# Performance work log

Hardware: AMD Instinct MI355X
Metric: run time of the kernel (lower is better)

The kernel has to match this reference:

```python
import jax, jax.numpy as jnp
import numpy as np
from jax import lax

B, C, H, W = 4, 256, 64, 64
R = 4  # reduction
BN_EPS = 1e-5


def setup_inputs() -> dict:
    key = jax.random.key(0)
    ks = jax.random.split(key, 18)
    n = jax.random.normal
    return {
        "x_self": n(ks[0], (B, C, H, W), jnp.float32),
        "x_other": n(ks[1], (B, C, H, W), jnp.float32),
        "q_w": n(ks[2], (C, C), jnp.float32) * 0.05,      # self_q 1x1 conv
        "q_b": n(ks[3], (C,), jnp.float32) * 0.05,
        "kv_w": n(ks[4], (2 * C, C), jnp.float32) * 0.05,  # other_kv 1x1 conv
        "kv_b": n(ks[5], (2 * C,), jnp.float32) * 0.05,
        "g1_w": n(ks[6], (C // R, C), jnp.float32) * 0.05,  # gate conv1
        "g1_b": n(ks[7], (C // R,), jnp.float32) * 0.05,
        "g2_w": n(ks[8], (1, C // R), jnp.float32) * 0.05,  # gate conv2
        "g2_b": n(ks[9], (1,), jnp.float32) * 0.05,
        "dw_w": n(ks[10], (C, 1, 3, 3), jnp.float32) * 0.1,  # depthwise 3x3
        "dw_b": n(ks[11], (C,), jnp.float32) * 0.05,
        "bn_g": jnp.ones((C,), jnp.float32),
        "bn_b": jnp.zeros((C,), jnp.float32),
        "bn_m": n(ks[12], (C,), jnp.float32) * 0.05,
        "bn_v": jax.random.uniform(ks[13], (C,), jnp.float32, 0.5, 1.5),
        "out_w": n(ks[14], (C, C), jnp.float32) * 0.05,
        "out_b": n(ks[15], (C,), jnp.float32) * 0.05,
    }


def _conv1x1(x, w, b):
    return jnp.einsum('bchw,oc->bohw', x, w) + b[None, :, None, None]


def reference(x_self, x_other, q_w, q_b, kv_w, kv_b, g1_w, g1_b, g2_w, g2_b,
              dw_w, dw_b, bn_g, bn_b, bn_m, bn_v, out_w, out_b):
    # local branch: depthwise 3x3 conv -> BatchNorm (eval stats) -> SiLU
    y = lax.conv_general_dilated(
        x_self, dw_w, (1, 1), 'SAME',
        feature_group_count=C,
        dimension_numbers=('NCHW', 'OIHW', 'NCHW')) + dw_b[None, :, None, None]
    scale = (bn_g / jnp.sqrt(bn_v + BN_EPS))[None, :, None, None]
    y = (y - bn_m[None, :, None, None]) * scale + bn_b[None, :, None, None]
    local_feat = y * jax.nn.sigmoid(y)  # SiLU

    # cross attention over HW tokens
    q = _conv1x1(x_self, q_w, q_b).reshape(B, C, H * W)
    kv = _conv1x1(x_other, kv_w, kv_b)
    k = kv[:, :C].reshape(B, C, H * W)
    v = kv[:, C:].reshape(B, C, H * W)
    attn = jnp.einsum('bcn,bcm->bnm', q, k) / jnp.sqrt(jnp.float32(C))  # [B,HW,HW]
    attn = jax.nn.softmax(attn, axis=-1)
    attn_out = jnp.einsum('bnm,bcm->bcn', attn, v).reshape(B, C, H, W)

    # channel-squeeze gate on x_self -> scalar per sample
    p = jnp.mean(x_self, axis=(2, 3))                 # [B,C] global avg pool
    g = jax.nn.relu(p @ g1_w.T + g1_b)                # [B,C//R]
    g = jax.nn.sigmoid(g @ g2_w.T + g2_b)             # [B,1]
    gate = g[:, :, None, None]

    fused = local_feat + gate * attn_out
    return _conv1x1(fused, out_w, out_b)
```

## Files before the change

### kernel.cpp

```cpp
#include <hip/hip_runtime.h>
#include <stdint.h>

#define BB 4
#define CC 256
#define HH 64
#define WWD 64
#define NN 4096
#define LOG2E 1.4426950408889634f

typedef __attribute__((ext_vector_type(8))) short short8;
typedef __attribute__((ext_vector_type(4))) float f32x4;
typedef __attribute__((ext_vector_type(16))) float f32x16;
typedef __attribute__((ext_vector_type(4))) unsigned short us4;
typedef unsigned long long ull;

__device__ __forceinline__ unsigned short f2bf(float f) {
  unsigned int u = __float_as_uint(f);
  u += 0x7fffu + ((u >> 16) & 1u);
  return (unsigned short)(u >> 16);
}
__device__ __forceinline__ float bf2f(unsigned short h) {
  return __uint_as_float(((unsigned int)h) << 16);
}
__device__ __forceinline__ short8 ld8(const unsigned short* p) {
  return *reinterpret_cast<const short8*>(p);
}
__device__ __forceinline__ unsigned char f2fp8(float v) {
  return (unsigned char)__builtin_amdgcn_cvt_pk_fp8_f32(v, v, 0, false);
}
__device__ __forceinline__ int rowmap(int reg, int h) {
  return (reg & 3) + 8 * (reg >> 2) + 4 * h;
}
__device__ __forceinline__ void gll16(const void* g, void* l) {
  __builtin_amdgcn_global_load_lds(
      (const __attribute__((address_space(1))) unsigned int*)g,
      (__attribute__((address_space(3))) unsigned int*)l, 16, 0, 0);
}

__global__ __launch_bounds__(256, 2) void k_pre(
    const float* __restrict__ xs, const float* __restrict__ xo,
    const float* __restrict__ dww, const float* __restrict__ dwb,
    const float* __restrict__ bng, const float* __restrict__ bnb,
    const float* __restrict__ bnm, const float* __restrict__ bnv,
    const float* __restrict__ qw, const float* __restrict__ kvw,
    const float* __restrict__ ow, unsigned short* __restrict__ XtS,
    unsigned short* __restrict__ XtO, unsigned short* __restrict__ localT,
    float* __restrict__ psumA, unsigned short* __restrict__ Wb) {
  __shared__ float rb3[3][64][67];
  __shared__ unsigned short sb[64][67];
  int tid = threadIdx.x;
  if (blockIdx.z == 8) {
    int i = (blockIdx.x * 64 + blockIdx.y) * 1024 + tid * 4;
    const float* src;
    if (i < 65536) src = qw + i;
    else if (i < 196608) src = kvw + (i - 65536);
    else src = ow + (i - 196608);
    f32x4 v = *reinterpret_cast<const f32x4*>(src);
    us4 r;
#pragma unroll
    for (int j = 0; j < 4; ++j) r[j] = f2bf(v[j]);
    *reinterpret_cast<us4*>(Wb + i) = r;
    return;
  }
  int c0 = blockIdx.x * 64, h = blockIdx.y;
  int b = blockIdx.z >> 1, which = blockIdx.z & 1;
  const float* src = which ? xo : xs;
  int wq = tid >> 6, w = tid & 63;
  int dlo = which ? 1 : 0, dhi = which ? 1 : 2;
  for (int d = dlo; d <= dhi; ++d) {
    int hh = h + d - 1;
    bool ok = (hh >= 0 && hh < HH);
#pragma unroll
    for (int p = 0; p < 4; ++p) {
      int idx = p * 256 + tid;
      int cl = idx >> 4, ws4 = (idx & 15) * 4;
      f32x4 v = {};
      if (ok)
        v = *reinterpret_cast<const f32x4*>(
            &src[(((size_t)(b * CC + c0 + cl)) * HH + hh) * WWD + ws4]);
#pragma unroll
      for (int j = 0; j < 4; ++j) rb3[d][cl][ws4 + 1 + j] = v[j];
    }
    if (tid < 64) { rb3[d][tid][0] = 0.f; rb3[d][tid][65] = 0.f; }
  }
  __syncthreads();
  unsigned short* dst = which ? XtO : XtS;
  int n0 = h * 64, cb = (tid & 15) * 4;
#pragma unroll
  for (int i = 0; i < 4; ++i) {
    int wl = i * 16 + (tid >> 4);
    us4 r;
#pragma unroll
    for (int j = 0; j < 4; ++j) r[j] = f2bf(rb3[1][cb + j][wl + 1]);
    *reinterpret_cast<us4*>(&dst[((size_t)b * NN + n0 + wl) * CC + c0 + cb]) = r;
  }
  if (which) return;
  if (tid < 64) {
    float s = 0.f;
    for (int ww = 0; ww < 64; ++ww) s += rb3[1][tid][ww + 1];
    psumA[((size_t)(b * 64 + h)) * CC + c0 + tid] = s;
  }
  for (int p = 0; p < 16; ++p) {
    int cl = p * 4 + wq, c = c0 + cl;
    float acc = 0.f;
#pragma unroll
    for (int di = 0; di < 3; ++di)
#pragma unroll
      for (int dj = 0; dj < 3; ++dj)
        acc = fmaf(rb3[di][cl][w + dj], dww[c * 9 + di * 3 + dj], acc);
    float y = acc + dwb[c];
    float sc = bng[c] * rsqrtf(bnv[c] + 1e-5f);
    float v = (y - bnm[c]) * sc + bnb[c];
    sb[cl][w] = f2bf(v / (1.f + __expf(-v)));
  }
  __syncthreads();
#pragma unroll
  for (int i = 0; i < 4; ++i) {
    int wl = i * 16 + (tid >> 4);
    us4 r;
#pragma unroll
    for (int j = 0; j < 4; ++j) r[j] = sb[cb + j][wl];
    *reinterpret_cast<us4*>(&localT[((size_t)b * NN + h * WWD + wl) * CC + c0 + cb]) = r;
  }
}

__global__ __launch_bounds__(256, 4) void k_qkv(
    const unsigned short* __restrict__ XtS, const unsigned short* __restrict__ XtO,
    const unsigned short* __restrict__ Wb, const float* __restrict__ qb,
    const float* __restrict__ kvb, const float* __restrict__ psumA,
    const float* __restrict__ g1w, const float* __restrict__ g1b,
    const float* __restrict__ g2w, const float* __restrict__ g2b,
    unsigned char* __restrict__ Qt8, unsigned char* __restrict__ Kt8,
    unsigned char* __restrict__ Vv8, float* __restrict__ gate) {
  __shared__ unsigned short Xs[64][264];
  int tid = threadIdx.x;
  int id = blockIdx.y;
  if (id == 3) {
    if (blockIdx.x != 0 || blockIdx.z != 0) return;
    float* mf = (float*)&Xs[0][0];
    float* hpf = mf + 1024;
    int c = tid;
    for (int b4 = 0; b4 < 4; ++b4) {
      float s = 0.f;
      for (int hh = 0; hh < 64; ++hh) s += psumA[((size_t)(b4 * 64 + hh)) * CC + c];
      mf[b4 * 256 + c] = s * (1.f / 4096.f);
    }
    __syncthreads();
    for (int b4 = 0; b4 < 4; ++b4) {
      int j = tid >> 2, cq = tid & 3;
      float s = 0.f;
      for (int cc = cq * 64; cc < cq * 64 + 64; ++cc)
        s = fmaf(mf[b4 * 256 + cc], g1w[j * CC + cc], s);
      hpf[j * 5 + cq] = s;
      __syncthreads();
      if (tid < 64) {
        float hh = fmaxf(hpf[tid * 5] + hpf[tid * 5 + 1] + hpf[tid * 5 + 2] +
                             hpf[tid * 5 + 3] + g1b[tid], 0.f);
        float t = hh * g2w[tid];
        for (int off = 32; off; off >>= 1) t += __shfl_down(t, off, 64);
        if (tid == 0) gate[b4] = 1.f / (1.f + expf(-(t + g2b[0])));
      }
      __syncthreads();
    }
    return;
  }
  int n0 = blockIdx.x * 64, b = blockIdx.z;
  const unsigned short* Xt = (id == 0) ? XtS : XtO;
  const unsigned short* W = Wb + id * 65536;
  int wave = tid >> 6, lane = tid & 63, l31 = lane & 31, h = lane >> 5;
#pragma unroll
  for (int p = 0; p < 8; ++p) {
    int r = p * 8 + (tid >> 5), c = (tid & 31) * 8;
    *reinterpret_cast<uint4*>(&Xs[r][c]) =
        *reinterpret_cast<const uint4*>(Xt + ((size_t)b * NN + n0 + r) * CC + c);
  }
  __syncthreads();
  int o0 = wave * 64;
  f32x16 acc[4] = {};
  if (id < 2) {
#pragma unroll
    for (int t = 0; t < 16; ++t) {
      short8 a0 = ld8(&Xs[l31][t * 16 + h * 8]);
      short8 a1 = ld8(&Xs[32 + l31][t * 16 + h * 8]);
      short8 b0 = ld8(W + (size_t)(o0 + l31) * CC + t * 16 + h * 8);
      short8 b1 = ld8(W + (size_t)(o0 + 32 + l31) * CC + t * 16 + h * 8);
      acc[0] = __builtin_amdgcn_mfma_f32_32x32x16_bf16(a0, b0, acc[0], 0, 0, 0);
      acc[1] = __builtin_amdgcn_mfma_f32_32x32x16_bf16(a0, b1, acc[1], 0, 0, 0);
      acc[2] = __builtin_amdgcn_mfma_f32_32x32x16_bf16(a1, b0, acc[2], 0, 0, 0);
      acc[3] = __builtin_amdgcn_mfma_f32_32x32x16_bf16(a1, b1, acc[3], 0, 0, 0);
    }
    const float* bias = id ? kvb : qb;
    unsigned char* Out8 = id ? Kt8 : Qt8;
    __syncthreads();
    unsigned char (*T8)[264] = reinterpret_cast<unsigned char(*)[264]>(&Xs[0][0]);
#pragma unroll
    for (int nt = 0; nt < 2; ++nt)
#pragma unroll
      for (int ot = 0; ot < 2; ++ot) {
        int o = o0 + ot * 32 + l31;
        float bv = bias[o];
#pragma unroll
        for (int reg = 0; reg < 16; ++reg) {
          int nl = nt * 32 + rowmap(reg, h);
          T8[nl][o] = f2fp8((acc[nt * 2 + ot][reg] + bv) * 0.25f);
        }
      }
    __syncthreads();
#pragma unroll
    for (int p = 0; p < 4; ++p) {
      int idx = p * 256 + tid, row = idx >> 4, cc = (idx & 15) * 16;
      int s = (id == 1) ? ((row & 31) << 3) : 0;
      ull a0 = *reinterpret_cast<const ull*>(&T8[row][cc ^ s]);
      ull a1 = *reinterpret_cast<const ull*>(&T8[row][(cc + 8) ^ s]);
      uint4 u;
      u.x = (unsigned)a0; u.y = (unsigned)(a0 >> 32);
      u.z = (unsigned)a1; u.w = (unsigned)(a1 >> 32);
      *reinterpret_cast<uint4*>(Out8 + ((size_t)b * NN + n0 + row) * CC + cc) = u;
    }
  } else {
#pragma unroll
    for (int t = 0; t < 16; ++t) {
      short8 a0 = ld8(W + (size_t)(o0 + l31) * CC + t * 16 + h * 8);
      short8 a1 = ld8(W + (size_t)(o0 + 32 + l31) * CC + t * 16 + h * 8);
      short8 b0 = ld8(&Xs[l31][t * 16 + h * 8]);
      short8 b1 = ld8(&Xs[32 + l31][t * 16 + h * 8]);
      acc[0] = __builtin_amdgcn_mfma_f32_32x32x16_bf16(a0, b0, acc[0], 0, 0, 0);
      acc[1] = __builtin_amdgcn_mfma_f32_32x32x16_bf16(a0, b1, acc[1], 0, 0, 0);
      acc[2] = __builtin_amdgcn_mfma_f32_32x32x16_bf16(a1, b0, acc[2], 0, 0, 0);
      acc[3] = __builtin_amdgcn_mfma_f32_32x32x16_bf16(a1, b1, acc[3], 0, 0, 0);
    }
    __syncthreads();
    unsigned char (*V8)[72] = reinterpret_cast<unsigned char(*)[72]>(&Xs[0][0]);
#pragma unroll
    for (int ot = 0; ot < 2; ++ot)
#pragma unroll
      for (int nt = 0; nt < 2; ++nt)
#pragma unroll
        for (int reg = 0; reg < 16; ++reg) {
          int o = o0 + ot * 32 + rowmap(reg, h);
          int nl = nt * 32 + l31;
          V8[o][nl] = f2fp8(acc[ot * 2 + nt][reg] + kvb[CC + o]);
        }
    __syncthreads();
#pragma unroll
    for (int p = 0; p < 4; ++p) {
      int idx = p * 256 + tid, o = idx >> 2, mm = (idx & 3) * 16;
      int s = ((o >> 1) & 7) << 3;
      ull a0 = *reinterpret_cast<const ull*>(&V8[o][mm ^ s]);
      ull a1 = *reinterpret_cast<const ull*>(&V8[o][(mm + 8) ^ s]);
      uint4 u;
      u.x = (unsigned)a0; u.y = (unsigned)(a0 >> 32);
      u.z = (unsigned)a1; u.w = (unsigned)(a1 >> 32);
      *reinterpret_cast<uint4*>(Vv8 + ((size_t)b * CC + o) * NN + n0 + mm) = u;
    }
  }
}

__global__ __launch_bounds__(256, 3) void k_flash8(
    const unsigned char* __restrict__ Qt8, const unsigned char* __restrict__ Kt8,
    const unsigned char* __restrict__ Vv8, const unsigned short* __restrict__ localT,
    const float* __restrict__ gate, unsigned short* __restrict__ OpartA,
    unsigned short* __restrict__ OpartB,
    float* __restrict__ Lpart, unsigned short* __restrict__ fusedT) {
  __shared__ unsigned char Ks8[64][256];
  __shared__ unsigned char Vs8[256][64];
  __shared__ unsigned char Ps8[64][72];
  __shared__ float lred[2][64];
  int b = blockIdx.x & 3, n0 = (blockIdx.x >> 2) * 64;
  int sp = blockIdx.y, nsp = gridDim.y;
  int tid = threadIdx.x, wave = tid >> 6, lane = tid & 63, l31 = lane & 31, h = lane >> 5;
  int rw = wave & 1, cw = wave >> 1;
  int wbase = tid & ~63;
  const unsigned char* qp = Qt8 + ((size_t)b * NN + n0 + rw * 32 + l31) * CC + h * 8;
  long qf[16];
#pragma unroll
  for (int t = 0; t < 16; ++t) qf[t] = *reinterpret_cast<const long*>(qp + t * 16);
  f32x16 O[4] = {};
  float lsumA = 0.f, lsumB = 0.f;
  int m_lo = (64 * sp) / nsp, m_hi = (64 * (sp + 1)) / nsp;
  const unsigned char* Kbase = Kt8 + (size_t)b * NN * CC;
  const unsigned char* Vbase = Vv8 + (size_t)b * CC * NN;
  {
    const unsigned char* Kg = Kbase + (size_t)(m_lo * 64) * CC;
#pragma unroll
    for (int p = 0; p < 4; ++p)
      gll16(Kg + (size_t)(p * 256 + tid) * 16, &Ks8[0][0] + (p * 256 + wbase) * 16);
  }
  const unsigned char* Krow = &Ks8[cw * 32 + l31][0];
  int ksw = l31 << 3;
  int vsw = ((l31 >> 1) & 7) << 3;
  for (int mt = m_lo; mt < m_hi; ++mt) {
    asm volatile("s_waitcnt vmcnt(0)" ::: "memory");
    __builtin_amdgcn_s_barrier();
    __builtin_amdgcn_sched_barrier(0);
    {
      const unsigned char* Vg = Vbase + mt * 64;
#pragma unroll
      for (int p = 0; p < 4; ++p) {
        int idx = p * 256 + tid;
        int c = idx >> 2, mm = (idx & 3) * 16;
        gll16(Vg + (size_t)c * NN + mm, &Vs8[0][0] + (p * 256 + wbase) * 16);
      }
    }
    __builtin_amdgcn_sched_barrier(0);
    f32x16 Sa = {}, Sb = {};
    __builtin_amdgcn_s_setprio(1);
#pragma unroll
    for (int t = 0; t < 8; ++t) {
      long kfa = *reinterpret_cast<const long*>(Krow + ((t * 16 + h * 8) ^ ksw));
      long kfb = *reinterpret_cast<const long*>(Krow + (((t + 8) * 16 + h * 8) ^ ksw));
      Sa = __builtin_amdgcn_mfma_f32_32x32x16_fp8_fp8(kfa, qf[t], Sa, 0, 0, 0);
      Sb = __builtin_amdgcn_mfma_f32_32x32x16_fp8_fp8(kfb, qf[t + 8], Sb, 0, 0, 0);
    }
    __builtin_amdgcn_s_setprio(0);
#pragma unroll
    for (int r = 0; r < 4; ++r) {
      float p0 = __builtin_exp2f((Sa[4 * r + 0] + Sb[4 * r + 0]) * LOG2E);
      float p1 = __builtin_exp2f((Sa[4 * r + 1] + Sb[4 * r + 1]) * LOG2E);
      float p2 = __builtin_exp2f((Sa[4 * r + 2] + Sb[4 * r + 2]) * LOG2E);
      float p3 = __builtin_exp2f((Sa[4 * r + 3] + Sb[4 * r + 3]) * LOG2E);
      lsumA += p0 + p1;
      lsumB += p2 + p3;
      unsigned u = __builtin_amdgcn_cvt_pk_fp8_f32(p0, p1, 0, false);
      u = __builtin_amdgcn_cvt_pk_fp8_f32(p2, p3, u, true);
      *reinterpret_cast<unsigned*>(&Ps8[rw * 32 + l31][cw * 32 + 8 * r + 4 * h]) = u;
    }
    asm volatile("s_waitcnt lgkmcnt(0)" ::: "memory");
    __builtin_amdgcn_s_barrier();
    __builtin_amdgcn_sched_barrier(0);
    {
      int mn = (mt + 1 < m_hi) ? mt + 1 : mt;
      const unsigned char* Kg = Kbase + (size_t)(mn * 64) * CC;
#pragma unroll
      for (int p = 0; p < 4; ++p)
        gll16(Kg + (size_t)(p * 256 + tid) * 16, &Ks8[0][0] + (p * 256 + wbase) * 16);
    }
    __builtin_amdgcn_sched_barrier(0);
    asm volatile("s_waitcnt vmcnt(4)" ::: "memory");
    __builtin_amdgcn_sched_barrier(0);
    __builtin_amdgcn_s_setprio(1);
#pragma unroll
    for (int t = 0; t < 4; ++t) {
      long pf = *reinterpret_cast<const long*>(&Ps8[rw * 32 + l31][t * 16 + h * 8]);
#pragma unroll
      for (int ct = 0; ct < 4; ++ct) {
        long vf = *reinterpret_cast<const long*>(
            &Vs8[cw * 128 + ct * 32 + l31][(t * 16 + h * 8) ^ vsw]);
        O[ct] = __builtin_amdgcn_mfma_f32_32x32x16_fp8_fp8(pf, vf, O[ct], 0, 0, 0);
      }
    }
    __builtin_amdgcn_s_setprio(0);
  }
  asm volatile("s_waitcnt vmcnt(0)" ::: "memory");
  float lsum = lsumA + lsumB;
  lsum += __shfl_xor(lsum, 32, 64);
  __syncthreads();
  if (h == 0) lred[cw][rw * 32 + l31] = lsum;
  __syncthreads();
  if (nsp == 1) {
    float* ltot = reinterpret_cast<float*>(&Ps8[0][0]);
    if (tid < 64) ltot[tid] = lred[0][tid] + lred[1][tid];
    __syncthreads();
    float gv = gate[b];
    float inv[16];
#pragma unroll
    for (int reg = 0; reg < 16; ++reg)
      inv[reg] = gv / ltot[rw * 32 + rowmap(reg, h)];
#pragma unroll
    for (int ct = 0; ct < 4; ++ct)
#pragma unroll
      for (int reg = 0; reg < 16; ++reg) {
        int n = n0 + rw * 32 + rowmap(reg, h);
        int c = cw * 128 + ct * 32 + l31;
        size_t idx = ((size_t)b * NN + n) * CC + c;
        fusedT[idx] = f2bf(bf2f(localT[idx]) + O[ct][reg] * inv[reg]);
      }
  } else {
    if (tid < 64) Lpart[(size_t)(b * nsp + sp) * NN + n0 + tid] = lred[0][tid] + lred[1][tid];
    unsigned short* Op;
    size_t slab;
    if (sp == 0) { Op = OpartA; slab = (size_t)b * NN; }
    else { Op = OpartB; slab = (size_t)(b * (nsp - 1) + (sp - 1)) * NN; }
#pragma unroll
    for (int ct = 0; ct < 4; ++ct)
#pragma unroll
      for (int reg = 0; reg < 16; ++reg) {
        int n = n0 + rw * 32 + rowmap(reg, h);
        int c = cw * 128 + ct * 32 + l31;
        Op[(slab + n) * CC + c] = f2bf(O[ct][reg]);
      }
  }
}

__global__ __launch_bounds__(256, 4) void k_out(
    const unsigned short* __restrict__ W, const float* __restrict__ ob,
    const float* __restrict__ gate, const unsigned short* __restrict__ localT,
    const unsigned short* __restrict__ OpartA, const unsigned short* __restrict__ OpartB,
    const float* __restrict__ Lpart,
    const unsigned short* __restrict__ fusedT, float* __restrict__ out, int nsp) {
  __shared__ unsigned short Xs[64][264];
  int n0 = blockIdx.x * 64, o0 = blockIdx.y * 128, b = blockIdx.z;
  int tid = threadIdx.x, wave = tid >> 6, lane = tid & 63, l31 = lane & 31, h = lane >> 5;
  if (nsp > 1) {
    float gv = gate[b];
#pragma unroll
    for (int p = 0; p < 8; ++p) {
      int r = p * 8 + (tid >> 5), cc = (tid & 31) * 8;
      int n = n0 + r;
      float lsum = 0.f;
      for (int sp = 0; sp < nsp; ++sp) lsum += Lpart[(size_t)(b * nsp + sp) * NN + n];
      float g = gv / lsum;
      float ov[8] = {};
      for (int sp = 0; sp < nsp; ++sp) {
        const unsigned short* Op;
        size_t slab;
        if (sp == 0) { Op = OpartA; slab = (size_t)b * NN; }
        else { Op = OpartB; slab = (size_t)(b * (nsp - 1) + (sp - 1)) * NN; }
        short8 x = ld8(Op + (slab + n) * CC + cc);
#pragma unroll
        for (int j = 0; j < 8; ++j) ov[j] += bf2f(((unsigned short*)&x)[j]);
      }
      const unsigned short* lp = localT + ((size_t)b * NN + n) * CC + cc;
      short8 lv = ld8(lp);
      us4 r0, r1;
#pragma unroll
      for (int j = 0; j < 4; ++j) {
        r0[j] = f2bf(bf2f(((unsigned short*)&lv)[j]) + ov[j] * g);
        r1[j] = f2bf(bf2f(((unsigned short*)&lv)[j + 4]) + ov[j + 4] * g);
      }
      *reinterpret_cast<us4*>(&Xs[r][cc]) = r0;
      *reinterpret_cast<us4*>(&Xs[r][cc + 4]) = r1;
    }
  } else {
#pragma unroll
    for (int p = 0; p < 8; ++p) {
      int r = p * 8 + (tid >> 5), c = (tid & 31) * 8;
      *reinterpret_cast<uint4*>(&Xs[r][c]) =
          *reinterpret_cast<const uint4*>(fusedT + ((size_t)b * NN + n0 + r) * CC + c);
    }
  }
  int obase = o0 + wave * 32;
  short8 af[16];
#pragma unroll
  for (int t = 0; t < 16; ++t) af[t] = ld8(W + (size_t)(obase + l31) * CC + t * 16 + h * 8);
  __syncthreads();
  f32x16 acc[2] = {};
#pragma unroll
  for (int t = 0; t < 16; ++t) {
    short8 b0 = ld8(&Xs[l31][t * 16 + h * 8]);
    short8 b1 = ld8(&Xs[32 + l31][t * 16 + h * 8]);
    acc[0] = __builtin_amdgcn_mfma_f32_32x32x16_bf16(af[t], b0, acc[0], 0, 0, 0);
    acc[1] = __builtin_amdgcn_mfma_f32_32x32x16_bf16(af[t], b1, acc[1], 0, 0, 0);
  }
#pragma unroll
  for (int nt = 0; nt < 2; ++nt)
#pragma unroll
    for (int reg = 0; reg < 16; ++reg) {
      int o = obase + rowmap(reg, h);
      int n = n0 + nt * 32 + l31;
      out[((size_t)b * CC + o) * NN + n] = acc[nt][reg] + ob[o];
    }
}

extern "C" void kernel_launch(void* const* d_in, const int* in_sizes, int n_in,
                              void* d_out, int out_size, void* d_ws, size_t ws_size,
                              hipStream_t stream) {
  const float* xs  = (const float*)d_in[0];
  const float* xo  = (const float*)d_in[1];
  const float* qw  = (const float*)d_in[2];
  const float* qb  = (const float*)d_in[3];
  const float* kvw = (const float*)d_in[4];
  const float* kvb = (const float*)d_in[5];
  const float* g1w = (const float*)d_in[6];
  const float* g1b = (const float*)d_in[7];
  const float* g2w = (const float*)d_in[8];
  const float* g2b = (const float*)d_in[9];
  const float* dww = (const float*)d_in[10];
  const float* dwb = (const float*)d_in[11];
  const float* bng = (const float*)d_in[12];
  const float* bnb = (const float*)d_in[13];
  const float* bnm = (const float*)d_in[14];
  const float* bnv = (const float*)d_in[15];
  const float* ow  = (const float*)d_in[16];
  const float* ob  = (const float*)d_in[17];
  float* out = (float*)d_out;
  char* ws = (char*)d_ws;

  const size_t SZ  = (size_t)BB * NN * CC * 2;
  const size_t SZ8 = (size_t)BB * NN * CC;
  unsigned short* XtS    = (unsigned short*)(ws);
  unsigned short* XtO    = (unsigned short*)(ws + SZ);
  unsigned short* localT = (unsigned short*)(ws + 2 * SZ);
  unsigned char*  Qt8    = (unsigned char*)(ws + 3 * SZ);
  unsigned char*  Kt8    = (unsigned char*)(ws + 3 * SZ + SZ8);
  unsigned char*  Vv8    = (unsigned char*)(ws + 3 * SZ + 2 * SZ8);
  unsigned short* Wb     = (unsigned short*)(ws + 3 * SZ + 3 * SZ8);
  float* psumA = (float*)(ws + 3 * SZ + 3 * SZ8 + 524288);
  float* gate  = (float*)(ws + 3 * SZ + 3 * SZ8 + 524288 + 262144);
  size_t tail  = 3 * SZ + 3 * SZ8 + 524288 + 262144 + 4096;
  float* Lpart = (float*)(ws + tail);
  unsigned short* OpartA = XtO;
  unsigned short* OpartB = (unsigned short*)(ws + tail + 262144);
  unsigned short* fusedT = XtS;

  size_t base = tail + 262144;
  int S = 1;
  if (ws_size >= base + 2ull * SZ) S = 3;
  else if (ws_size >= base + 1ull * SZ) S = 2;

  k_pre<<<dim3(4, 64, 9), 256, 0, stream>>>(xs, xo, dww, dwb, bng, bnb, bnm, bnv,
                                            qw, kvw, ow, XtS, XtO, localT, psumA, Wb);
  k_qkv<<<dim3(64, 4, 4), 256, 0, stream>>>(XtS, XtO, Wb, qb, kvb, psumA,
                                            g1w, g1b, g2w, g2b, Qt8, Kt8, Vv8, gate);
  k_flash8<<<dim3(256, S), 256, 0, stream>>>(Qt8, Kt8, Vv8, localT, gate, OpartA,
                                             OpartB, Lpart, fusedT);
  k_out<<<dim3(64, 2, 4), 256, 0, stream>>>(Wb + 196608, ob, gate, localT,
                                            OpartA, OpartB, Lpart, fusedT, out, S);
}
```

Before: 248.4 us.

## Pre-tile K/V into MFMA fragment order and load directly from global in flash kernel

The projection kernel now writes K and V in a blocked layout where each lane's 8-byte MFMA operand is contiguous and adjacent lanes are adjacent in memory. The attention kernel drops its LDS staging of K/V tiles (global_load_lds, swizzles, waitcnt pipelining) and reads fragments straight from global memory. Key tiles are widened from 64 to 128 keys per iteration, which halves the loop count and barriers. In exchange it relies on L2/cache bandwidth with no explicit prefetch overlap, so the global load latency may be exposed.

New measurement: 250.9 us. No clear change (+1.0%).

```diff
diff --git a/kernel.cpp b/kernel.cpp
--- a/kernel.cpp
+++ b/kernel.cpp
@@ -30,11 +30,6 @@
 }
 __device__ __forceinline__ int rowmap(int reg, int h) {
   return (reg & 3) + 8 * (reg >> 2) + 4 * h;
-}
-__device__ __forceinline__ void gll16(const void* g, void* l) {
-  __builtin_amdgcn_global_load_lds(
-      (const __attribute__((address_space(1))) unsigned int*)g,
-      (__attribute__((address_space(3))) unsigned int*)l, 16, 0, 0);
 }
 
 __global__ __launch_bounds__(256, 2) void k_pre(
@@ -190,7 +185,6 @@
       acc[3] = __builtin_amdgcn_mfma_f32_32x32x16_bf16(a1, b1, acc[3], 0, 0, 0);
     }
     const float* bias = id ? kvb : qb;
-    unsigned char* Out8 = id ? Kt8 : Qt8;
     __syncthreads();
     unsigned char (*T8)[264] = reinterpret_cast<unsigned char(*)[264]>(&Xs[0][0]);
 #pragma unroll
@@ -206,16 +200,26 @@
         }
       }
     __syncthreads();
-#pragma unroll
-    for (int p = 0; p < 4; ++p) {
-      int idx = p * 256 + tid, row = idx >> 4, cc = (idx & 15) * 16;
-      int s = (id == 1) ? ((row & 31) << 3) : 0;
-      ull a0 = *reinterpret_cast<const ull*>(&T8[row][cc ^ s]);
-      ull a1 = *reinterpret_cast<const ull*>(&T8[row][(cc + 8) ^ s]);
-      uint4 u;
-      u.x = (unsigned)a0; u.y = (unsigned)(a0 >> 32);
-      u.z = (unsigned)a1; u.w = (unsigned)(a1 >> 32);
-      *reinterpret_cast<uint4*>(Out8 + ((size_t)b * NN + n0 + row) * CC + cc) = u;
+    if (id == 0) {
+#pragma unroll
+      for (int p = 0; p < 4; ++p) {
+        int idx = p * 256 + tid, row = idx >> 4, cc = (idx & 15) * 16;
+        ull a0 = *reinterpret_cast<const ull*>(&T8[row][cc]);
+        ull a1 = *reinterpret_cast<const ull*>(&T8[row][cc + 8]);
+        uint4 u;
+        u.x = (unsigned)a0; u.y = (unsigned)(a0 >> 32);
+        u.z = (unsigned)a1; u.w = (unsigned)(a1 >> 32);
+        *reinterpret_cast<uint4*>(Qt8 + ((size_t)b * NN + n0 + row) * CC + cc) = u;
+      }
+    } else {
+      size_t tb = ((size_t)b * 32 + (n0 >> 7)) * 32768 + (size_t)(n0 & 64) * 8;
+#pragma unroll
+      for (int p = 0; p < 8; ++p) {
+        int ch = p * 256 + tid;
+        int m = ch & 63, s2 = ch >> 6;
+        *reinterpret_cast<ull*>(Kt8 + tb + (size_t)s2 * 1024 + m * 8) =
+            *reinterpret_cast<const ull*>(&T8[m][s2 * 8]);
+      }
     }
   } else {
 #pragma unroll
@@ -242,117 +246,86 @@
           V8[o][nl] = f2fp8(acc[ot * 2 + nt][reg] + kvb[CC + o]);
         }
     __syncthreads();
-#pragma unroll
-    for (int p = 0; p < 4; ++p) {
-      int idx = p * 256 + tid, o = idx >> 2, mm = (idx & 3) * 16;
-      int s = ((o >> 1) & 7) << 3;
-      ull a0 = *reinterpret_cast<const ull*>(&V8[o][mm ^ s]);
-      ull a1 = *reinterpret_cast<const ull*>(&V8[o][(mm + 8) ^ s]);
-      uint4 u;
-      u.x = (unsigned)a0; u.y = (unsigned)(a0 >> 32);
-      u.z = (unsigned)a1; u.w = (unsigned)(a1 >> 32);
-      *reinterpret_cast<uint4*>(Vv8 + ((size_t)b * CC + o) * NN + n0 + mm) = u;
+    size_t tb = ((size_t)b * 32 + (n0 >> 7)) * 32768 + (size_t)((n0 & 64) >> 3) * 2048;
+#pragma unroll
+    for (int p = 0; p < 8; ++p) {
+      int ch = p * 256 + tid;
+      int c = ch & 255, svl = ch >> 8;
+      *reinterpret_cast<ull*>(Vv8 + tb + (size_t)svl * 2048 + c * 8) =
+          *reinterpret_cast<const ull*>(&V8[c][svl * 8]);
     }
   }
 }
 
 __global__ __launch_bounds__(256, 3) void k_flash8(
-    const unsigned char* __restrict__ Qt8, const unsigned char* __restrict__ Kt8,
-    const unsigned char* __restrict__ Vv8, const unsigned short* __restrict__ localT,
+    const unsigned char* __restrict__ Qt8, const unsigned char* __restrict__ Kd,
+    const unsigned char* __restrict__ Vd, const unsigned short* __restrict__ localT,
     const float* __restrict__ gate, unsigned short* __restrict__ OpartA,
     unsigned short* __restrict__ OpartB,
     float* __restrict__ Lpart, unsigned short* __restrict__ fusedT) {
-  __shared__ unsigned char Ks8[64][256];
-  __shared__ unsigned char Vs8[256][64];
-  __shared__ unsigned char Ps8[64][72];
+  __shared__ unsigned char Ps8[64][136];
   __shared__ float lred[2][64];
   int b = blockIdx.x & 3, n0 = (blockIdx.x >> 2) * 64;
   int sp = blockIdx.y, nsp = gridDim.y;
   int tid = threadIdx.x, wave = tid >> 6, lane = tid & 63, l31 = lane & 31, h = lane >> 5;
   int rw = wave & 1, cw = wave >> 1;
-  int wbase = tid & ~63;
   const unsigned char* qp = Qt8 + ((size_t)b * NN + n0 + rw * 32 + l31) * CC + h * 8;
   long qf[16];
 #pragma unroll
   for (int t = 0; t < 16; ++t) qf[t] = *reinterpret_cast<const long*>(qp + t * 16);
   f32x16 O[4] = {};
-  float lsumA = 0.f, lsumB = 0.f;
-  int m_lo = (64 * sp) / nsp, m_hi = (64 * (sp + 1)) / nsp;
-  const unsigned char* Kbase = Kt8 + (size_t)b * NN * CC;
-  const unsigned char* Vbase = Vv8 + (size_t)b * CC * NN;
-  {
-    const unsigned char* Kg = Kbase + (size_t)(m_lo * 64) * CC;
-#pragma unroll
-    for (int p = 0; p < 4; ++p)
-      gll16(Kg + (size_t)(p * 256 + tid) * 16, &Ks8[0][0] + (p * 256 + wbase) * 16);
-  }
-  const unsigned char* Krow = &Ks8[cw * 32 + l31][0];
-  int ksw = l31 << 3;
-  int vsw = ((l31 >> 1) & 7) << 3;
+  float lsum = 0.f;
+  int m_lo = (32 * sp) / nsp, m_hi = (32 * (sp + 1)) / nsp;
+  const unsigned char* Kb = Kd + (size_t)b * (32u * 32768u);
+  const unsigned char* Vb = Vd + (size_t)b * (32u * 32768u);
   for (int mt = m_lo; mt < m_hi; ++mt) {
-    asm volatile("s_waitcnt vmcnt(0)" ::: "memory");
-    __builtin_amdgcn_s_barrier();
-    __builtin_amdgcn_sched_barrier(0);
-    {
-      const unsigned char* Vg = Vbase + mt * 64;
-#pragma unroll
-      for (int p = 0; p < 4; ++p) {
-        int idx = p * 256 + tid;
-        int c = idx >> 2, mm = (idx & 3) * 16;
-        gll16(Vg + (size_t)c * NN + mm, &Vs8[0][0] + (p * 256 + wbase) * 16);
-      }
-    }
-    __builtin_amdgcn_sched_barrier(0);
+    const unsigned char* Kq = Kb + (size_t)mt * 32768 + h * 1024 + (cw * 64 + l31) * 8;
     f32x16 Sa = {}, Sb = {};
     __builtin_amdgcn_s_setprio(1);
 #pragma unroll
-    for (int t = 0; t < 8; ++t) {
-      long kfa = *reinterpret_cast<const long*>(Krow + ((t * 16 + h * 8) ^ ksw));
-      long kfb = *reinterpret_cast<const long*>(Krow + (((t + 8) * 16 + h * 8) ^ ksw));
+    for (int t = 0; t < 16; ++t) {
+      long kfa = *reinterpret_cast<const long*>(Kq + (size_t)t * 2048);
+      long kfb = *reinterpret_cast<const long*>(Kq + (size_t)t * 2048 + 256);
       Sa = __builtin_amdgcn_mfma_f32_32x32x16_fp8_fp8(kfa, qf[t], Sa, 0, 0, 0);
-      Sb = __builtin_amdgcn_mfma_f32_32x32x16_fp8_fp8(kfb, qf[t + 8], Sb, 0, 0, 0);
+      Sb = __builtin_amdgcn_mfma_f32_32x32x16_fp8_fp8(kfb, qf[t], Sb, 0, 0, 0);
     }
     __builtin_amdgcn_s_setprio(0);
 #pragma unroll
     for (int r = 0; r < 4; ++r) {
-      float p0 = __builtin_exp2f((Sa[4 * r + 0] + Sb[4 * r + 0]) * LOG2E);
-      float p1 = __builtin_exp2f((Sa[4 * r + 1] + Sb[4 * r + 1]) * LOG2E);
-      float p2 = __builtin_exp2f((Sa[4 * r + 2] + Sb[4 * r + 2]) * LOG2E);
-      float p3 = __builtin_exp2f((Sa[4 * r + 3] + Sb[4 * r + 3]) * LOG2E);
-      lsumA += p0 + p1;
-      lsumB += p2 + p3;
+      float p0 = __builtin_exp2f(Sa[4 * r + 0] * LOG2E);
+      float p1 = __builtin_exp2f(Sa[4 * r + 1] * LOG2E);
+      float p2 = __builtin_exp2f(Sa[4 * r + 2] * LOG2E);
+      float p3 = __builtin_exp2f(Sa[4 * r + 3] * LOG2E);
+      lsum += (p0 + p1) + (p2 + p3);
       unsigned u = __builtin_amdgcn_cvt_pk_fp8_f32(p0, p1, 0, false);
       u = __builtin_amdgcn_cvt_pk_fp8_f32(p2, p3, u, true);
-      *reinterpret_cast<unsigned*>(&Ps8[rw * 32 + l31][cw * 32 + 8 * r + 4 * h]) = u;
+      *reinterpret_cast<unsigned*>(&Ps8[rw * 32 + l31][cw * 64 + 8 * r + 4 * h]) = u;
+      float q0 = __builtin_exp2f(Sb[4 * r + 0] * LOG2E);
+      float q1 = __builtin_exp2f(Sb[4 * r + 1] * LOG2E);
+      float q2 = __builtin_exp2f(Sb[4 * r + 2] * LOG2E);
+      float q3 = __builtin_exp2f(Sb[4 * r + 3] * LOG2E);
+      lsum += (q0 + q1) + (q2 + q3);
+      unsigned u2 = __builtin_amdgcn_cvt_pk_fp8_f32(q0, q1, 0, false);
+      u2 = __builtin_amdgcn_cvt_pk_fp8_f32(q2, q3, u2, true);
+      *reinterpret_cast<unsigned*>(&Ps8[rw * 32 + l31][cw * 64 + 32 + 8 * r + 4 * h]) = u2;
     }
     asm volatile("s_waitcnt lgkmcnt(0)" ::: "memory");
     __builtin_amdgcn_s_barrier();
     __builtin_amdgcn_sched_barrier(0);
-    {
-      int mn = (mt + 1 < m_hi) ? mt + 1 : mt;
-      const unsigned char* Kg = Kbase + (size_t)(mn * 64) * CC;
-#pragma unroll
-      for (int p = 0; p < 4; ++p)
-        gll16(Kg + (size_t)(p * 256 + tid) * 16, &Ks8[0][0] + (p * 256 + wbase) * 16);
-    }
-    __builtin_amdgcn_sched_barrier(0);
-    asm volatile("s_waitcnt vmcnt(4)" ::: "memory");
-    __builtin_amdgcn_sched_barrier(0);
+    const unsigned char* Vq = Vb + (size_t)mt * 32768 + h * 2048 + (cw * 128 + l31) * 8;
     __builtin_amdgcn_s_setprio(1);
 #pragma unroll
-    for (int t = 0; t < 4; ++t) {
+    for (int t = 0; t < 8; ++t) {
       long pf = *reinterpret_cast<const long*>(&Ps8[rw * 32 + l31][t * 16 + h * 8]);
 #pragma unroll
       for (int ct = 0; ct < 4; ++ct) {
-        long vf = *reinterpret_cast<const long*>(
-            &Vs8[cw * 128 + ct * 32 + l31][(t * 16 + h * 8) ^ vsw]);
+        long vf = *reinterpret_cast<const long*>(Vq + (size_t)t * 4096 + ct * 256);
         O[ct] = __builtin_amdgcn_mfma_f32_32x32x16_fp8_fp8(pf, vf, O[ct], 0, 0, 0);
       }
     }
     __builtin_amdgcn_s_setprio(0);
-  }
-  asm volatile("s_waitcnt vmcnt(0)" ::: "memory");
-  float lsum = lsumA + lsumB;
+    __builtin_amdgcn_s_barrier();
+  }
   lsum += __shfl_xor(lsum, 32, 64);
   __syncthreads();
   if (h == 0) lred[cw][rw * 32 + l31] = lsum;
```
